# Optimization experiments

Measured on AMD Instinct MI355X. Metric: run time of the kernel, lower is better.

Reference implementation:

```python
import jax, jax.numpy as jnp
import numpy as np


def setup_inputs() -> dict:
    key = jax.random.key(0)
    k1, k2 = jax.random.split(key)
    B, D, S = 8, 64, 512
    x = jax.random.normal(k1, (B, D, S), dtype=jnp.float32)
    # bracket_products[0]: bias-free Linear(2*D -> D); stored as (2*D, D), applied feat @ W
    W = jax.random.normal(k2, (2 * D, D), dtype=jnp.float32) * (1.0 / np.sqrt(2 * D))
    return {"x": x, "W": W}


def reference(x, W):
    # x: (B, D, S); W: (2D, D)
    B, D, S = x.shape
    # torch builds y_out[b, :, i, j] = concat(x[b,:,j], x[b,:,i]) for i >= j (tril), zeros elsewhere,
    # then applies Linear(2D->D). Split W so the full linear is a broadcast sum of two per-position
    # projections, avoiding the explicit (B, 2D, S, S) scatter.
    W_w, W_h = W[:D], W[D:]                      # x_w part (col j), x_h part (row i)
    a = jnp.einsum('bdj,dk->bjk', x, W_w)        # (B, S, D): column-j contribution
    b = jnp.einsum('bdi,dk->bik', x, W_h)        # (B, S, D): row-i contribution
    mask = jnp.tril(jnp.ones((S, S), dtype=x.dtype))  # rows i >= cols j
    # pair[b,i,j,k] == bracket linear output at (row i, col j); zero on strict upper triangle
    pair = (a[:, None, :, :] + b[:, :, None, :]) * mask[None, :, :, None]  # (B, S, S, D)
    n = jnp.linalg.norm(pair, axis=-1)           # L2 over channel dim -> (B, S, S)
    wmat = 1.0 - n                                # upper triangle: 1 - 0 = 1, matching torch
    # torch: einsum('bdw,bdwi->bdi', x, weight) with weight (B,1,S,S) broadcast over d
    c = jnp.einsum('bdw,bwi->bdi', x, wmat)       # contract over row index w
    return c
```

## Files before the change

### kernel.cpp

```cpp
#include <hip/hip_runtime.h>
#include <math.h>

#define NB 8
#define ND 64
#define NS 512

typedef __attribute__((ext_vector_type(8))) short bf16x8;
typedef __attribute__((ext_vector_type(4))) float f32x4;
typedef __attribute__((ext_vector_type(4))) unsigned short us4;
typedef __attribute__((ext_vector_type(8))) unsigned short us8;

__device__ __forceinline__ unsigned short f2bf(float f) {
    unsigned int u = __float_as_uint(f);
    unsigned int r = (u + 0x7FFFu + ((u >> 16) & 1u)) >> 16;
    return (unsigned short)r;
}

#define MFMA __builtin_amdgcn_mfma_f32_16x16x32_bf16

__global__ __launch_bounds__(256) void k_part(const float* __restrict__ x,
                                              const float* __restrict__ W,
                                              float* __restrict__ part) {
    __shared__ __align__(16) unsigned short WT[128 * 64];
    __shared__ __align__(16) unsigned short xwd_i[64 * 64];
    __shared__ __align__(16) unsigned short xwd_u[64 * 64];
    __shared__ __align__(16) unsigned short xdw[64 * 64];
    __shared__ __align__(16) unsigned short alds[64 * 64];
    __shared__ __align__(16) unsigned short blds[64 * 64];
    __shared__ __align__(16) unsigned short wmb[64 * 64];
    __shared__ float na_lds[64], nb_lds[64];

    int b = blockIdx.y;
    int v = blockIdx.x;
    int u = 0;
    while ((u + 1) * (u + 2) / 2 <= v) ++u;
    int ti = v - u * (u + 1) / 2;
    int i0 = ti * 64, w0 = u * 64;

    int t = threadIdx.x;
    int lane = t & 63, wv = t >> 6, c = lane & 15, g = lane >> 4, c7 = c & 7;

    {
        int n = t & 127, half = t >> 7;
#pragma unroll
        for (int p = 0; p < 4; ++p) {
            int dg = half * 4 + p;
            us8 h;
#pragma unroll
            for (int dd = 0; dd < 8; ++dd)
                h[dd] = f2bf(W[(size_t)(dg * 8 + dd) * ND + (n & 63) + ((n >> 6) * (ND * ND))]);
            *(us8*)&WT[n * 64 + ((dg ^ (n & 7)) << 3)] = h;
        }
    }
    {
        int wl = t & 63, w2 = t >> 6;
#pragma unroll
        for (int j = 0; j < 2; ++j) {
            int dblk = 2 * w2 + j;
            us8 hi, hu;
#pragma unroll
            for (int e = 0; e < 8; ++e) {
                int d = 8 * dblk + e;
                const float* base = x + ((size_t)(b * ND) + d) * NS;
                hi[e] = f2bf(base[i0 + wl]);
                hu[e] = f2bf(base[w0 + wl]);
            }
            *(us8*)&xwd_i[wl * 64 + ((dblk ^ (wl & 7)) << 3)] = hi;
            *(us8*)&xwd_u[wl * 64 + ((dblk ^ (wl & 7)) << 3)] = hu;
        }
    }
#pragma unroll
    for (int q = 0; q < 2; ++q) {
        int e = t + 256 * q;
        int d = e >> 3, wc = e & 7;
        const float4* p4 = (const float4*)(x + ((size_t)(b * ND) + d) * NS + w0 + 8 * wc);
        float4 v0 = p4[0], v1 = p4[1];
        us8 h;
        h[0] = f2bf(v0.x); h[1] = f2bf(v0.y); h[2] = f2bf(v0.z); h[3] = f2bf(v0.w);
        h[4] = f2bf(v1.x); h[5] = f2bf(v1.y); h[6] = f2bf(v1.z); h[7] = f2bf(v1.w);
        *(us8*)&xdw[d * 64 + ((wc ^ (d & 7)) << 3)] = h;
    }
    __syncthreads();

    {
        f32x4 aacc[4] = {{0,0,0,0},{0,0,0,0},{0,0,0,0},{0,0,0,0}};
        f32x4 bacc[4] = {{0,0,0,0},{0,0,0,0},{0,0,0,0},{0,0,0,0}};
#pragma unroll
        for (int ks = 0; ks < 2; ++ks) {
            int row = 16 * wv + c;
            bf16x8 Pi = *(const bf16x8*)&xwd_i[row * 64 + (((4 * ks + g) ^ c7) << 3)];
            bf16x8 Pu = *(const bf16x8*)&xwd_u[row * 64 + (((4 * ks + g) ^ c7) << 3)];
#pragma unroll
            for (int qb = 0; qb < 4; ++qb) {
                bf16x8 Qw = *(const bf16x8*)&WT[(16 * qb + c) * 64 + (((4 * ks + g) ^ c7) << 3)];
                bf16x8 Qh = *(const bf16x8*)&WT[(64 + 16 * qb + c) * 64 + (((4 * ks + g) ^ c7) << 3)];
                aacc[qb] = MFMA(Pi, Qw, aacc[qb], 0, 0, 0);
                bacc[qb] = MFMA(Pu, Qh, bacc[qb], 0, 0, 0);
            }
        }
#pragma unroll
        for (int r = 0; r < 4; ++r) {
            float sa = aacc[0][r] * aacc[0][r] + aacc[1][r] * aacc[1][r]
                     + aacc[2][r] * aacc[2][r] + aacc[3][r] * aacc[3][r];
            float sb = bacc[0][r] * bacc[0][r] + bacc[1][r] * bacc[1][r]
                     + bacc[2][r] * bacc[2][r] + bacc[3][r] * bacc[3][r];
            sa += __shfl_xor(sa, 1, 64); sa += __shfl_xor(sa, 2, 64);
            sa += __shfl_xor(sa, 4, 64); sa += __shfl_xor(sa, 8, 64);
            sb += __shfl_xor(sb, 1, 64); sb += __shfl_xor(sb, 2, 64);
            sb += __shfl_xor(sb, 4, 64); sb += __shfl_xor(sb, 8, 64);
            if (c == 0) {
                na_lds[16 * wv + 4 * g + r] = sa;
                nb_lds[16 * wv + 4 * g + r] = sb;
            }
        }
#pragma unroll
        for (int qb = 0; qb < 4; ++qb)
#pragma unroll
            for (int r = 0; r < 4; ++r) {
                int row = 16 * wv + 4 * g + r, k = 16 * qb + c;
                int off = row * 64 + (((k >> 3) ^ (row & 7)) << 3) + (k & 7);
                alds[off] = f2bf(aacc[qb][r]);
                blds[off] = f2bf(bacc[qb][r]);
            }
    }
    __syncthreads();

    {
        int wrow = 16 * wv + c;
        bf16x8 P0 = *(const bf16x8*)&blds[wrow * 64 + ((g ^ c7) << 3)];
        bf16x8 P1 = *(const bf16x8*)&blds[wrow * 64 + (((4 + g) ^ c7) << 3)];
        float nbv[4];
#pragma unroll
        for (int r = 0; r < 4; ++r) nbv[r] = nb_lds[16 * wv + 4 * g + r];
        int wbase = w0 + 16 * wv + 4 * g;
#pragma unroll
        for (int n = 0; n < 4; ++n) {
            int arow = 16 * n + c;
            f32x4 a1 = {0.f, 0.f, 0.f, 0.f};
            bf16x8 Q0 = *(const bf16x8*)&alds[arow * 64 + ((g ^ c7) << 3)];
            bf16x8 Q1 = *(const bf16x8*)&alds[arow * 64 + (((4 + g) ^ c7) << 3)];
            a1 = MFMA(P0, Q0, a1, 0, 0, 0);
            a1 = MFMA(P1, Q1, a1, 0, 0, 0);
            float navv = na_lds[arow];
            int i_glob = i0 + arow;
            us4 pk;
#pragma unroll
            for (int r = 0; r < 4; ++r) {
                float s2v = navv + nbv[r] + 2.f * a1[r];
                float val = (i_glob <= wbase + r) ? -sqrtf(fmaxf(s2v, 0.f)) : 0.f;
                pk[r] = f2bf(val);
            }
            int wblk = 2 * wv + (g >> 1);
            *(us4*)&wmb[arow * 64 + ((wblk ^ (arow & 7)) << 3) + 4 * (g & 1)] = pk;
        }
    }
    __syncthreads();

    {
        int il = 16 * wv + c;
        bf16x8 a20 = *(const bf16x8*)&wmb[il * 64 + ((g ^ c7) << 3)];
        bf16x8 a21 = *(const bf16x8*)&wmb[il * 64 + (((4 + g) ^ c7) << 3)];
#pragma unroll
        for (int nd = 0; nd < 4; ++nd) {
            int d = 16 * nd + c;
            bf16x8 q0 = *(const bf16x8*)&xdw[d * 64 + ((g ^ c7) << 3)];
            bf16x8 q1 = *(const bf16x8*)&xdw[d * 64 + (((4 + g) ^ c7) << 3)];
            f32x4 acc = {0.f, 0.f, 0.f, 0.f};
            acc = MFMA(a20, q0, acc, 0, 0, 0);
            acc = MFMA(a21, q1, acc, 0, 0, 0);
            float* pp = part + (((size_t)u * NB + b) * ND + d) * NS + i0 + 16 * wv + 4 * g;
            *(f32x4*)pp = acc;
        }
    }
}

__global__ __launch_bounds__(256) void k_red(const float* __restrict__ x,
                                             const float* __restrict__ part,
                                             float* __restrict__ out) {
    __shared__ float red[4];
    int b = blockIdx.y, d = blockIdx.x, t = threadIdx.x;
    const float* xr = x + ((size_t)b * ND + d) * NS;

    float s = xr[t] + xr[t + 256];
#pragma unroll
    for (int m = 32; m >= 1; m >>= 1) s += __shfl_xor(s, m, 64);
    if ((t & 63) == 0) red[t >> 6] = s;
    __syncthreads();
    float rs = red[0] + red[1] + red[2] + red[3];

#pragma unroll
    for (int q = 0; q < 2; ++q) {
        int i  = t + q * 256;
        int it = i >> 6;
        float vv = rs;
#pragma unroll
        for (int u = 0; u < 8; ++u) {
            if (u >= it)
                vv += part[(((size_t)u * NB + b) * ND + d) * NS + i];
        }
        out[((size_t)b * ND + d) * NS + i] = vv;
    }
}

extern "C" void kernel_launch(void* const* d_in, const int* in_sizes, int n_in,
                              void* d_out, int out_size, void* d_ws, size_t ws_size,
                              hipStream_t stream) {
    const float* x = (const float*)d_in[0];
    const float* W = (const float*)d_in[1];
    float* out  = (float*)d_out;
    float* part = (float*)d_ws;

    k_part<<<dim3(36, NB), dim3(256), 0, stream>>>(x, W, part);
    k_red <<<dim3(ND, NB), dim3(256), 0, stream>>>(x, part, out);
}
```

Baseline: 19.86 us.

## Batch global loads before conversion in k_part and vectorize k_red with float4

In k_part, all global loads of x and W are issued into registers up front, and the bf16 conversions and LDS stores happen afterwards. This lets more loads be in flight at once instead of serializing load-convert-store, and launch bounds now request 2 blocks per CU. In k_red, the block size drops to 128 threads, and each thread handles 4 consecutive outputs with float4 loads of x and part and a float4 store, which cuts instruction count and per-element address math. The cost is higher register pressure in k_part, and the occupancy hint may force spills.

```diff
diff --git a/kernel.cpp b/kernel.cpp
--- a/kernel.cpp
+++ b/kernel.cpp
@@ -18,9 +18,9 @@
 
 #define MFMA __builtin_amdgcn_mfma_f32_16x16x32_bf16
 
-__global__ __launch_bounds__(256) void k_part(const float* __restrict__ x,
-                                              const float* __restrict__ W,
-                                              float* __restrict__ part) {
+__global__ __launch_bounds__(256, 2) void k_part(const float* __restrict__ x,
+                                                 const float* __restrict__ W,
+                                                 float* __restrict__ part) {
     __shared__ __align__(16) unsigned short WT[128 * 64];
     __shared__ __align__(16) unsigned short xwd_i[64 * 64];
     __shared__ __align__(16) unsigned short xwd_u[64 * 64];
@@ -40,45 +40,67 @@
     int t = threadIdx.x;
     int lane = t & 63, wv = t >> 6, c = lane & 15, g = lane >> 4, c7 = c & 7;
 
-    {
-        int n = t & 127, half = t >> 7;
-#pragma unroll
-        for (int p = 0; p < 4; ++p) {
-            int dg = half * 4 + p;
-            us8 h;
-#pragma unroll
-            for (int dd = 0; dd < 8; ++dd)
-                h[dd] = f2bf(W[(size_t)(dg * 8 + dd) * ND + (n & 63) + ((n >> 6) * (ND * ND))]);
-            *(us8*)&WT[n * 64 + ((dg ^ (n & 7)) << 3)] = h;
-        }
-    }
-    {
-        int wl = t & 63, w2 = t >> 6;
-#pragma unroll
-        for (int j = 0; j < 2; ++j) {
-            int dblk = 2 * w2 + j;
-            us8 hi, hu;
-#pragma unroll
-            for (int e = 0; e < 8; ++e) {
-                int d = 8 * dblk + e;
-                const float* base = x + ((size_t)(b * ND) + d) * NS;
-                hi[e] = f2bf(base[i0 + wl]);
-                hu[e] = f2bf(base[w0 + wl]);
-            }
-            *(us8*)&xwd_i[wl * 64 + ((dblk ^ (wl & 7)) << 3)] = hi;
-            *(us8*)&xwd_u[wl * 64 + ((dblk ^ (wl & 7)) << 3)] = hu;
-        }
-    }
+    int wl = t & 63, w2 = t >> 6;
+    float xi_[16], xu_[16];
+#pragma unroll
+    for (int j = 0; j < 2; ++j)
+#pragma unroll
+        for (int e = 0; e < 8; ++e) {
+            int d = 8 * (2 * w2 + j) + e;
+            const float* base = x + ((size_t)(b * ND) + d) * NS;
+            xi_[8 * j + e] = base[i0 + wl];
+            xu_[8 * j + e] = base[w0 + wl];
+        }
+    float4 xd_[4];
 #pragma unroll
     for (int q = 0; q < 2; ++q) {
         int e = t + 256 * q;
         int d = e >> 3, wc = e & 7;
         const float4* p4 = (const float4*)(x + ((size_t)(b * ND) + d) * NS + w0 + 8 * wc);
-        float4 v0 = p4[0], v1 = p4[1];
+        xd_[2 * q]     = p4[0];
+        xd_[2 * q + 1] = p4[1];
+    }
+#pragma unroll
+    for (int j = 0; j < 2; ++j) {
+        int dblk = 2 * w2 + j;
+        us8 hi, hu;
+#pragma unroll
+        for (int e = 0; e < 8; ++e) {
+            hi[e] = f2bf(xi_[8 * j + e]);
+            hu[e] = f2bf(xu_[8 * j + e]);
+        }
+        *(us8*)&xwd_i[wl * 64 + ((dblk ^ (wl & 7)) << 3)] = hi;
+        *(us8*)&xwd_u[wl * 64 + ((dblk ^ (wl & 7)) << 3)] = hu;
+    }
+#pragma unroll
+    for (int q = 0; q < 2; ++q) {
+        int e = t + 256 * q;
+        int d = e >> 3, wc = e & 7;
+        float4 v0 = xd_[2 * q], v1 = xd_[2 * q + 1];
         us8 h;
         h[0] = f2bf(v0.x); h[1] = f2bf(v0.y); h[2] = f2bf(v0.z); h[3] = f2bf(v0.w);
         h[4] = f2bf(v1.x); h[5] = f2bf(v1.y); h[6] = f2bf(v1.z); h[7] = f2bf(v1.w);
         *(us8*)&xdw[d * 64 + ((wc ^ (d & 7)) << 3)] = h;
+    }
+    {
+        int n = t & 127, half = t >> 7;
+        float wv_[32];
+#pragma unroll
+        for (int p = 0; p < 4; ++p)
+#pragma unroll
+            for (int dd = 0; dd < 8; ++dd) {
+                int dg = half * 4 + p;
+                wv_[8 * p + dd] =
+                    W[(size_t)(dg * 8 + dd) * ND + (n & 63) + ((n >> 6) * (ND * ND))];
+            }
+#pragma unroll
+        for (int p = 0; p < 4; ++p) {
+            int dg = half * 4 + p;
+            us8 h;
+#pragma unroll
+            for (int dd = 0; dd < 8; ++dd) h[dd] = f2bf(wv_[8 * p + dd]);
+            *(us8*)&WT[n * 64 + ((dg ^ (n & 7)) << 3)] = h;
+        }
     }
     __syncthreads();
 
@@ -174,32 +196,31 @@
     }
 }
 
-__global__ __launch_bounds__(256) void k_red(const float* __restrict__ x,
+__global__ __launch_bounds__(128) void k_red(const float* __restrict__ x,
                                              const float* __restrict__ part,
                                              float* __restrict__ out) {
-    __shared__ float red[4];
+    __shared__ float red[2];
     int b = blockIdx.y, d = blockIdx.x, t = threadIdx.x;
     const float* xr = x + ((size_t)b * ND + d) * NS;
 
-    float s = xr[t] + xr[t + 256];
+    float4 xv = *(const float4*)(xr + 4 * t);
+    float s = xv.x + xv.y + xv.z + xv.w;
 #pragma unroll
     for (int m = 32; m >= 1; m >>= 1) s += __shfl_xor(s, m, 64);
     if ((t & 63) == 0) red[t >> 6] = s;
     __syncthreads();
-    float rs = red[0] + red[1] + red[2] + red[3];
-
-#pragma unroll
-    for (int q = 0; q < 2; ++q) {
-        int i  = t + q * 256;
-        int it = i >> 6;
-        float vv = rs;
-#pragma unroll
-        for (int u = 0; u < 8; ++u) {
-            if (u >= it)
-                vv += part[(((size_t)u * NB + b) * ND + d) * NS + i];
-        }
-        out[((size_t)b * ND + d) * NS + i] = vv;
-    }
+    float rs = red[0] + red[1];
+
+    int it = t >> 4;
+    f32x4 vv = {rs, rs, rs, rs};
+#pragma unroll
+    for (int u = 0; u < 8; ++u) {
+        if (u >= it) {
+            f32x4 pv = *(const f32x4*)&part[(((size_t)u * NB + b) * ND + d) * NS + 4 * t];
+            vv[0] += pv[0]; vv[1] += pv[1]; vv[2] += pv[2]; vv[3] += pv[3];
+        }
+    }
+    *(f32x4*)&out[((size_t)b * ND + d) * NS + 4 * t] = vv;
 }
 
 extern "C" void kernel_launch(void* const* d_in, const int* in_sizes, int n_in,
@@ -211,5 +232,5 @@
     float* part = (float*)d_ws;
 
     k_part<<<dim3(36, NB), dim3(256), 0, stream>>>(x, W, part);
-    k_red <<<dim3(ND, NB), dim3(256), 0, stream>>>(x, part, out);
-}
+    k_red <<<dim3(ND, NB), dim3(128), 0, stream>>>(x, part, out);
+}
```

Result: faster. 18.65 us (-6.1%).
